# Kernel tuning notes

Hardware: AMD Instinct MI355X
Metric: run time of the kernel (lower is better)

Reference implementation:

```python
import jax, jax.numpy as jnp
import numpy as np

EMBED_DIM = 1024
NUM_HEADS = 16
HEAD_DIM = EMBED_DIM // NUM_HEADS
LN_EPS = 1e-5


def setup_inputs() -> dict:
    key = jax.random.key(0)
    ks = jax.random.split(key, 7)
    B, N, D = 4, 2048, EMBED_DIM
    s = 1.0 / np.sqrt(D)  # ~kaiming-uniform scale for Linear weights
    return {
        "inputs": jax.random.normal(ks[0], (B, N, D), dtype=jnp.float32),
        "W_q": jax.random.uniform(ks[1], (D, D), jnp.float32, -s, s),
        "W_k": jax.random.uniform(ks[2], (D, D), jnp.float32, -s, s),
        "W_v": jax.random.uniform(ks[3], (D, D), jnp.float32, -s, s),
        "W_o": jax.random.uniform(ks[4], (D, D), jnp.float32, -s, s),
        "ln_gamma": jnp.ones((D,), jnp.float32),
        "ln_beta": jnp.zeros((D,), jnp.float32),
    }


def reference(inputs, W_q, W_k, W_v, W_o, ln_gamma, ln_beta):
    x = inputs
    B, N, D = x.shape
    H, Hd = NUM_HEADS, HEAD_DIM
    # torch nn.Linear computes x @ W.T; W_* stored as (out, in)
    q = (x @ W_q.T).reshape(B, N, H, Hd).transpose(0, 2, 1, 3)  # [B,H,N,Hd]
    k = (x @ W_k.T).reshape(B, N, H, Hd).transpose(0, 2, 1, 3)
    v = (x @ W_v.T).reshape(B, N, H, Hd).transpose(0, 2, 1, 3)
    scores = jnp.einsum("bhqd,bhkd->bhqk", q, k) / jnp.sqrt(jnp.float32(Hd))
    attn = jax.nn.softmax(scores, axis=-1)  # dropout p=0 -> identity
    out = jnp.einsum("bhqk,bhkd->bhqd", attn, v)
    out = out.transpose(0, 2, 1, 3).reshape(B, N, D)
    out = out @ W_o.T
    # residual + LayerNorm
    y = out + x
    mu = jnp.mean(y, axis=-1, keepdims=True)
    var = jnp.mean(jnp.square(y - mu), axis=-1, keepdims=True)
    y = (y - mu) * jax.lax.rsqrt(var + LN_EPS)
    return y * ln_gamma + ln_beta
```

## Files before the change

### kernel.cpp

```cpp
#include <hip/hip_runtime.h>
#include <hip/hip_bf16.h>
#include <stdint.h>

typedef __attribute__((ext_vector_type(8))) short bf16x8;
typedef __attribute__((ext_vector_type(4))) float f32x4;

#define GLOBAL_AS __attribute__((address_space(1)))
#define LDS_AS    __attribute__((address_space(3)))

__device__ __forceinline__ void load_lds16(const void* g, void* l) {
  __builtin_amdgcn_global_load_lds((const GLOBAL_AS void*)g, (LDS_AS void*)l, 16, 0, 0);
}

__device__ __forceinline__ float bf2f(short s) {
  return __uint_as_float(((unsigned)(unsigned short)s) << 16);
}
__device__ __forceinline__ short f2bfn(float f) {
  __hip_bfloat16 h = __float2bfloat16(f);
  return __builtin_bit_cast(short, h);
}

__global__ __launch_bounds__(256) void cvt_bf16(const float* __restrict__ in,
                                                short* __restrict__ out, int n) {
  int i = (blockIdx.x * 256 + threadIdx.x) * 8;
  if (i >= n) return;
  float4 a = *(const float4*)(in + i);
  float4 b = *(const float4*)(in + i + 4);
  bf16x8 o;
  o[0] = f2bfn(a.x); o[1] = f2bfn(a.y); o[2] = f2bfn(a.z); o[3] = f2bfn(a.w);
  o[4] = f2bfn(b.x); o[5] = f2bfn(b.y); o[6] = f2bfn(b.z); o[7] = f2bfn(b.w);
  *(bf16x8*)(out + i) = o;
}

__global__ __launch_bounds__(256) void cvt_w(const float* __restrict__ q,
                                             const float* __restrict__ k,
                                             const float* __restrict__ v,
                                             const float* __restrict__ o,
                                             short* __restrict__ Wb,
                                             short* __restrict__ Wob) {
  const int sel = blockIdx.x >> 9;
  const int inner = blockIdx.x & 511;
  const int i = (inner * 256 + threadIdx.x) * 8;
  const float* src = sel == 0 ? q : sel == 1 ? k : sel == 2 ? v : o;
  short* dst = sel == 0 ? Wb : sel == 1 ? Wb + 1024 * 1024
             : sel == 2 ? Wb + 2 * 1024 * 1024 : Wob;
  float4 a = *(const float4*)(src + i);
  float4 b = *(const float4*)(src + i + 4);
  bf16x8 ov;
  ov[0] = f2bfn(a.x); ov[1] = f2bfn(a.y); ov[2] = f2bfn(a.z); ov[3] = f2bfn(a.w);
  ov[4] = f2bfn(b.x); ov[5] = f2bfn(b.y); ov[6] = f2bfn(b.z); ov[7] = f2bfn(b.w);
  *(bf16x8*)(dst + i) = ov;
}

template<int OUT_BF16>
__global__ __launch_bounds__(256) void gemm_bt(const short* __restrict__ A,
                                               const short* __restrict__ B,
                                               void* __restrict__ Cp,
                                               int M, int N, int K) {
  __shared__ short As[128 * 64];
  __shared__ short Bs[128 * 64];
  const int t = threadIdx.x, l = t & 63, w = t >> 6;
  const int g = l >> 4, li = l & 15;
  const int wr = w >> 1, wc = w & 1;
  const int bid = blockIdx.x;
  const int bm = (bid & 7) * 8 + ((bid >> 3) & 7);
  const int bn = bid >> 6;
  f32x4 acc[4][4] = {};
  const size_t arow0 = (size_t)(bm * 128) * K;
  const size_t brow0 = (size_t)(bn * 128) * K;
  for (int k0 = 0; k0 < K; k0 += 64) {
    __syncthreads();
#pragma unroll
    for (int it = 0; it < 4; ++it) {
      int e = it * 2048 + t * 8;
      int r = e >> 6, c = e & 63;
      load_lds16(A + arow0 + (size_t)r * K + (k0 + c), &As[e]);
      load_lds16(B + brow0 + (size_t)r * K + (k0 + c), &Bs[e]);
    }
    __syncthreads();
#pragma unroll
    for (int kk = 0; kk < 2; ++kk) {
      bf16x8 af[4], bfr[4];
#pragma unroll
      for (int m = 0; m < 4; ++m)
        af[m] = *(const bf16x8*)&As[(wr * 64 + m * 16 + li) * 64 + kk * 32 + g * 8];
#pragma unroll
      for (int n = 0; n < 4; ++n)
        bfr[n] = *(const bf16x8*)&Bs[(wc * 64 + n * 16 + li) * 64 + kk * 32 + g * 8];
#pragma unroll
      for (int m = 0; m < 4; ++m)
#pragma unroll
        for (int n = 0; n < 4; ++n)
          acc[m][n] = __builtin_amdgcn_mfma_f32_16x16x32_bf16(af[m], bfr[n], acc[m][n], 0, 0, 0);
    }
  }
#pragma unroll
  for (int m = 0; m < 4; ++m)
#pragma unroll
    for (int n = 0; n < 4; ++n)
#pragma unroll
      for (int r = 0; r < 4; ++r) {
        int row = bm * 128 + wr * 64 + m * 16 + g * 4 + r;
        int col = bn * 128 + wc * 64 + n * 16 + li;
        if (OUT_BF16)
          ((short*)Cp)[(size_t)row * N + col] = f2bfn(acc[m][n][r]);
        else
          ((float*)Cp)[(size_t)row * N + col] = acc[m][n][r];
      }
}

__global__ __launch_bounds__(256) void transpose_v(const short* __restrict__ qkv,
                                                   short* __restrict__ VT) {
  const int kt = blockIdx.x;
  const int bh = blockIdx.y;
  const int b = bh >> 4, h = bh & 15;
  __shared__ short T[64][72];
  const int t = threadIdx.x;
  const size_t src = (size_t)b * 2048 * 3072 + 2048 + (size_t)h * 64;
#pragma unroll
  for (int i = 0; i < 2; ++i) {
    int k = i * 32 + (t >> 3);
    int d0 = (t & 7) * 8;
    bf16x8 v = *(const bf16x8*)(qkv + src + (size_t)(kt * 64 + k) * 3072 + d0);
#pragma unroll
    for (int j = 0; j < 8; ++j) T[d0 + j][k] = v[j];
  }
  __syncthreads();
#pragma unroll
  for (int i = 0; i < 2; ++i) {
    int d = i * 32 + (t >> 3);
    int k0 = (t & 7) * 8;
    bf16x8 v = *(const bf16x8*)&T[d][k0];
    *(bf16x8*)(VT + ((size_t)bh * 64 + d) * 2048 + kt * 64 + k0) = v;
  }
}

__global__ __launch_bounds__(256, 4) void attn_fwd(const short* __restrict__ qkv,
                                                   const short* __restrict__ VT,
                                                   short* __restrict__ obuf) {
  const int f0 = blockIdx.x;
  const int work = (f0 & 7) * 128 + (f0 >> 3);
  const int qt = work & 15;
  const int bh = work >> 4;
  const int b = bh >> 4, h = bh & 15;
  const int t = threadIdx.x, w = t >> 6, l = t & 63;
  const int g = l >> 4, li = l & 15;

  __shared__ short Ks[2][64 * 64];
  __shared__ short Vts[2][64 * 64];
  __shared__ short Ps[4][16 * 64];

  const size_t base = (size_t)b * 2048 * 3072 + (size_t)h * 64;
  const short* Vsrc = VT + (size_t)bh * 64 * 2048;

  bf16x8 qf[2][2];
  {
    const float QSC = 0.125f * 1.44269504088896341f;
#pragma unroll
    for (int qh = 0; qh < 2; ++qh) {
      const short* qp = qkv + base + (size_t)(qt * 128 + w * 32 + qh * 16 + li) * 3072;
#pragma unroll
      for (int c = 0; c < 2; ++c) {
        bf16x8 v = *(const bf16x8*)(qp + c * 32 + g * 8);
#pragma unroll
        for (int i = 0; i < 8; ++i) v[i] = f2bfn(bf2f(v[i]) * QSC);
        qf[qh][c] = v;
      }
    }
  }

  bf16x8 ones;
#pragma unroll
  for (int i = 0; i < 8; ++i) ones[i] = (short)0x3F80;

  float m_[2] = {-1e30f, -1e30f};
  f32x4 o_[2][4], lacc[2];
#pragma unroll
  for (int qh = 0; qh < 2; ++qh) {
#pragma unroll
    for (int dj = 0; dj < 4; ++dj) o_[qh][dj] = (f32x4){0.f, 0.f, 0.f, 0.f};
    lacc[qh] = (f32x4){0.f, 0.f, 0.f, 0.f};
  }

  const int sw = li & 7;

#define STAGE(buf, kt_)                                                          \
  {                                                                              \
    _Pragma("unroll")                                                            \
    for (int it = 0; it < 2; ++it) {                                             \
      int e = it * 2048 + t * 8;                                                 \
      int r = e >> 6;                                                            \
      int cs = (e >> 3) & 7;                                                     \
      int cg = cs ^ (r & 7);                                                     \
      load_lds16(qkv + base + 1024 + (size_t)((kt_) * 64 + r) * 3072 + cg * 8,   \
                 &Ks[buf][e]);                                                   \
      load_lds16(Vsrc + (size_t)r * 2048 + (kt_) * 64 + cg * 8, &Vts[buf][e]);   \
    }                                                                            \
  }

  STAGE(0, 0);
  asm volatile("s_waitcnt vmcnt(0)" ::: "memory");
  __syncthreads();

  for (int kt = 0; kt < 32; ++kt) {
    const int cur = kt & 1;
    if (kt + 1 < 32) STAGE(cur ^ 1, kt + 1);

    f32x4 s_[2][4];
#pragma unroll
    for (int qh = 0; qh < 2; ++qh)
#pragma unroll
      for (int j = 0; j < 4; ++j) s_[qh][j] = (f32x4){0.f, 0.f, 0.f, 0.f};
    __builtin_amdgcn_s_setprio(1);
#pragma unroll
    for (int c = 0; c < 2; ++c)
#pragma unroll
      for (int j = 0; j < 4; ++j) {
        bf16x8 kf = *(const bf16x8*)&Ks[cur][(j * 16 + li) * 64 + (((c * 4 + g) ^ sw) * 8)];
        s_[0][j] = __builtin_amdgcn_mfma_f32_16x16x32_bf16(kf, qf[0][c], s_[0][j], 0, 0, 0);
        s_[1][j] = __builtin_amdgcn_mfma_f32_16x16x32_bf16(kf, qf[1][c], s_[1][j], 0, 0, 0);
      }
    __builtin_amdgcn_s_setprio(0);

    float mt[2];
#pragma unroll
    for (int qh = 0; qh < 2; ++qh) {
      float a0 = fmaxf(fmaxf(s_[qh][0][0], s_[qh][0][1]), s_[qh][0][2]);
      float a1 = fmaxf(fmaxf(s_[qh][0][3], s_[qh][1][0]), s_[qh][1][1]);
      float a2 = fmaxf(fmaxf(s_[qh][1][2], s_[qh][1][3]), s_[qh][2][0]);
      float a3 = fmaxf(fmaxf(s_[qh][2][1], s_[qh][2][2]), s_[qh][2][3]);
      float a4 = fmaxf(fmaxf(s_[qh][3][0], s_[qh][3][1]), s_[qh][3][2]);
      float b0 = fmaxf(fmaxf(a0, a1), a2);
      float b1 = fmaxf(fmaxf(a3, a4), s_[qh][3][3]);
      float m0 = fmaxf(b0, b1);
      m0 = fmaxf(m0, __shfl_xor(m0, 16));
      m0 = fmaxf(m0, __shfl_xor(m0, 32));
      mt[qh] = m0;
    }

    bool ok = (mt[0] <= m_[0] + 8.f) && (mt[1] <= m_[1] + 8.f);
    if (!__all(ok)) {
#pragma unroll
      for (int qh = 0; qh < 2; ++qh) {
        float mn = fmaxf(m_[qh], mt[qh]);
        float al = exp2f(m_[qh] - mn);
        m_[qh] = mn;
#pragma unroll
        for (int r = 0; r < 4; ++r) {
          float alr = __shfl(al, (l & 48) | (g * 4 + r));
#pragma unroll
          for (int dj = 0; dj < 4; ++dj) o_[qh][dj][r] *= alr;
          lacc[qh][r] *= alr;
        }
      }
    }

#pragma unroll
    for (int qh = 0; qh < 2; ++qh) {
#pragma unroll
      for (int j = 0; j < 4; ++j) {
        float p0 = exp2f(s_[qh][j][0] - m_[qh]);
        float p1 = exp2f(s_[qh][j][1] - m_[qh]);
        float p2 = exp2f(s_[qh][j][2] - m_[qh]);
        float p3 = exp2f(s_[qh][j][3] - m_[qh]);
        unsigned u0, u1;
        asm("v_cvt_pk_bf16_f32 %0, %1, %2" : "=v"(u0) : "v"(p0), "v"(p1));
        asm("v_cvt_pk_bf16_f32 %0, %1, %2" : "=v"(u1) : "v"(p2), "v"(p3));
        uint2 pk2; pk2.x = u0; pk2.y = u1;
        int pos = (j * 16 + g * 4) ^ (sw << 3);
        *(uint2*)&Ps[w][li * 64 + pos] = pk2;
      }
      asm volatile("s_waitcnt lgkmcnt(0)" ::: "memory");

      __builtin_amdgcn_s_setprio(1);
#pragma unroll
      for (int c = 0; c < 2; ++c) {
        bf16x8 pa = *(const bf16x8*)&Ps[w][li * 64 + (((c * 4 + g) ^ sw) * 8)];
        lacc[qh] = __builtin_amdgcn_mfma_f32_16x16x32_bf16(pa, ones, lacc[qh], 0, 0, 0);
#pragma unroll
        for (int dj = 0; dj < 4; ++dj) {
          bf16x8 vb = *(const bf16x8*)&Vts[cur][(dj * 16 + li) * 64 + (((c * 4 + g) ^ sw) * 8)];
          o_[qh][dj] = __builtin_amdgcn_mfma_f32_16x16x32_bf16(pa, vb, o_[qh][dj], 0, 0, 0);
        }
      }
      __builtin_amdgcn_s_setprio(0);
    }

    asm volatile("s_waitcnt vmcnt(0)" ::: "memory");
    __syncthreads();
  }

#pragma unroll
  for (int qh = 0; qh < 2; ++qh)
#pragma unroll
    for (int r = 0; r < 4; ++r) {
      float ilr = 1.f / lacc[qh][r];
      int row = b * 2048 + qt * 128 + w * 32 + qh * 16 + g * 4 + r;
#pragma unroll
      for (int dj = 0; dj < 4; ++dj) {
        int col = h * 64 + dj * 16 + li;
        obuf[(size_t)row * 1024 + col] = f2bfn(o_[qh][dj][r] * ilr);
      }
    }
#undef STAGE
}

__global__ __launch_bounds__(256) void resid_ln(const float* __restrict__ U,
                                                const float* __restrict__ x,
                                                const float* __restrict__ gamma,
                                                const float* __restrict__ beta,
                                                float* __restrict__ out) {
  const int row = blockIdx.x;
  const int t = threadIdx.x, w = t >> 6, l = t & 63;
  const float4 uu = *(const float4*)(U + (size_t)row * 1024 + t * 4);
  const float4 xx = *(const float4*)(x + (size_t)row * 1024 + t * 4);
  float y[4] = {uu.x + xx.x, uu.y + xx.y, uu.z + xx.z, uu.w + xx.w};
  float s = (y[0] + y[1]) + (y[2] + y[3]);
#pragma unroll
  for (int d = 1; d < 64; d <<= 1) s += __shfl_xor(s, d);
  __shared__ float red[4];
  if (l == 0) red[w] = s;
  __syncthreads();
  s = red[0] + red[1] + red[2] + red[3];
  const float mu = s * (1.f / 1024.f);
  float vs = 0.f;
#pragma unroll
  for (int i = 0; i < 4; ++i) { float d0 = y[i] - mu; vs += d0 * d0; }
#pragma unroll
  for (int d = 1; d < 64; d <<= 1) vs += __shfl_xor(vs, d);
  __syncthreads();
  if (l == 0) red[w] = vs;
  __syncthreads();
  vs = red[0] + red[1] + red[2] + red[3];
  const float rstd = rsqrtf(vs * (1.f / 1024.f) + 1e-5f);
  const float4 gg = *(const float4*)(gamma + t * 4);
  const float4 bb = *(const float4*)(beta + t * 4);
  float4 oo;
  oo.x = (y[0] - mu) * rstd * gg.x + bb.x;
  oo.y = (y[1] - mu) * rstd * gg.y + bb.y;
  oo.z = (y[2] - mu) * rstd * gg.z + bb.z;
  oo.w = (y[3] - mu) * rstd * gg.w + bb.w;
  *(float4*)(out + (size_t)row * 1024 + t * 4) = oo;
}

extern "C" void kernel_launch(void* const* d_in, const int* in_sizes, int n_in,
                              void* d_out, int out_size, void* d_ws, size_t ws_size,
                              hipStream_t stream) {
  const float* x     = (const float*)d_in[0];
  const float* W_q   = (const float*)d_in[1];
  const float* W_k   = (const float*)d_in[2];
  const float* W_v   = (const float*)d_in[3];
  const float* W_o   = (const float*)d_in[4];
  const float* gamma = (const float*)d_in[5];
  const float* beta  = (const float*)d_in[6];
  float* out = (float*)d_out;

  char* ws = (char*)d_ws;
  short* xb   = (short*)ws;  ws += (size_t)8192 * 1024 * 2;
  short* Wb   = (short*)ws;  ws += (size_t)3072 * 1024 * 2;
  short* Wob  = (short*)ws;  ws += (size_t)1024 * 1024 * 2;
  short* qkv  = (short*)ws;  ws += (size_t)8192 * 3072 * 2;
  short* obuf = (short*)ws;  ws += (size_t)8192 * 1024 * 2;
  float* U    = (float*)ws;  ws += (size_t)8192 * 1024 * 4;
  short* VT   = (short*)U;

  cvt_bf16<<<4096, 256, 0, stream>>>(x, xb, 8192 * 1024);
  cvt_w<<<2048, 256, 0, stream>>>(W_q, W_k, W_v, W_o, Wb, Wob);

  gemm_bt<1><<<1536, 256, 0, stream>>>(xb, Wb, qkv, 8192, 3072, 1024);
  transpose_v<<<dim3(32, 64), 256, 0, stream>>>(qkv, VT);
  attn_fwd<<<1024, 256, 0, stream>>>(qkv, VT, obuf);
  gemm_bt<0><<<512, 256, 0, stream>>>(obuf, Wob, U, 8192, 1024, 1024);
  resid_ln<<<8192, 256, 0, stream>>>(U, x, gamma, beta, out);
}
```

Measured before the change: 262.6 us.

## Load V fragments directly into registers and fold softmax scale into exp

V tiles are no longer staged through LDS. Each wave loads its V MFMA operands straight from global memory into registers at the start of each key tile, which removes the Vts shared buffer and halves LDS use. Separately, Q is no longer pre-scaled and re-rounded to bf16. The scale is applied with an fma inside the exp2 and in the rescale threshold. The trade-off is redundant global/L2 reads of V by all four waves, plus an earlier vmcnt(0) wait that also blocks on the next K prefetch.

After: 472.8 us. 1.8x slower.

```diff
diff --git a/kernel.cpp b/kernel.cpp
--- a/kernel.cpp
+++ b/kernel.cpp
@@ -147,27 +147,22 @@
   const int g = l >> 4, li = l & 15;
 
   __shared__ short Ks[2][64 * 64];
-  __shared__ short Vts[2][64 * 64];
   __shared__ short Ps[4][16 * 64];
 
   const size_t base = (size_t)b * 2048 * 3072 + (size_t)h * 64;
   const short* Vsrc = VT + (size_t)bh * 64 * 2048;
 
   bf16x8 qf[2][2];
-  {
-    const float QSC = 0.125f * 1.44269504088896341f;
-#pragma unroll
-    for (int qh = 0; qh < 2; ++qh) {
-      const short* qp = qkv + base + (size_t)(qt * 128 + w * 32 + qh * 16 + li) * 3072;
-#pragma unroll
-      for (int c = 0; c < 2; ++c) {
-        bf16x8 v = *(const bf16x8*)(qp + c * 32 + g * 8);
-#pragma unroll
-        for (int i = 0; i < 8; ++i) v[i] = f2bfn(bf2f(v[i]) * QSC);
-        qf[qh][c] = v;
-      }
-    }
-  }
+#pragma unroll
+  for (int qh = 0; qh < 2; ++qh) {
+    const short* qp = qkv + base + (size_t)(qt * 128 + w * 32 + qh * 16 + li) * 3072;
+#pragma unroll
+    for (int c = 0; c < 2; ++c)
+      qf[qh][c] = *(const bf16x8*)(qp + c * 32 + g * 8);
+  }
+
+  const float QSC = 0.125f * 1.44269504088896341f;
+  const float THR = 8.0f / QSC;
 
   bf16x8 ones;
 #pragma unroll
@@ -194,7 +189,6 @@
       int cg = cs ^ (r & 7);                                                     \
       load_lds16(qkv + base + 1024 + (size_t)((kt_) * 64 + r) * 3072 + cg * 8,   \
                  &Ks[buf][e]);                                                   \
-      load_lds16(Vsrc + (size_t)r * 2048 + (kt_) * 64 + cg * 8, &Vts[buf][e]);   \
     }                                                                            \
   }
 
@@ -204,6 +198,15 @@
 
   for (int kt = 0; kt < 32; ++kt) {
     const int cur = kt & 1;
+
+    bf16x8 vb[2][4];
+#pragma unroll
+    for (int c = 0; c < 2; ++c)
+#pragma unroll
+      for (int dj = 0; dj < 4; ++dj)
+        vb[c][dj] = *(const bf16x8*)(Vsrc + (size_t)(dj * 16 + li) * 2048 +
+                                     kt * 64 + c * 32 + g * 8);
+
     if (kt + 1 < 32) STAGE(cur ^ 1, kt + 1);
 
     f32x4 s_[2][4];
@@ -238,12 +241,12 @@
       mt[qh] = m0;
     }
 
-    bool ok = (mt[0] <= m_[0] + 8.f) && (mt[1] <= m_[1] + 8.f);
+    bool ok = (mt[0] <= m_[0] + THR) && (mt[1] <= m_[1] + THR);
     if (!__all(ok)) {
 #pragma unroll
       for (int qh = 0; qh < 2; ++qh) {
         float mn = fmaxf(m_[qh], mt[qh]);
-        float al = exp2f(m_[qh] - mn);
+        float al = exp2f((m_[qh] - mn) * QSC);
         m_[qh] = mn;
 #pragma unroll
         for (int r = 0; r < 4; ++r) {
@@ -257,12 +260,13 @@
 
 #pragma unroll
     for (int qh = 0; qh < 2; ++qh) {
+      const float mq = m_[qh] * QSC;
 #pragma unroll
       for (int j = 0; j < 4; ++j) {
-        float p0 = exp2f(s_[qh][j][0] - m_[qh]);
-        float p1 = exp2f(s_[qh][j][1] - m_[qh]);
-        float p2 = exp2f(s_[qh][j][2] - m_[qh]);
-        float p3 = exp2f(s_[qh][j][3] - m_[qh]);
+        float p0 = exp2f(fmaf(s_[qh][j][0], QSC, -mq));
+        float p1 = exp2f(fmaf(s_[qh][j][1], QSC, -mq));
+        float p2 = exp2f(fmaf(s_[qh][j][2], QSC, -mq));
+        float p3 = exp2f(fmaf(s_[qh][j][3], QSC, -mq));
         unsigned u0, u1;
         asm("v_cvt_pk_bf16_f32 %0, %1, %2" : "=v"(u0) : "v"(p0), "v"(p1));
         asm("v_cvt_pk_bf16_f32 %0, %1, %2" : "=v"(u1) : "v"(p2), "v"(p3));
@@ -271,6 +275,7 @@
         *(uint2*)&Ps[w][li * 64 + pos] = pk2;
       }
       asm volatile("s_waitcnt lgkmcnt(0)" ::: "memory");
+      if (qh == 0) asm volatile("s_waitcnt vmcnt(0)" ::: "memory");
 
       __builtin_amdgcn_s_setprio(1);
 #pragma unroll
@@ -278,15 +283,12 @@
         bf16x8 pa = *(const bf16x8*)&Ps[w][li * 64 + (((c * 4 + g) ^ sw) * 8)];
         lacc[qh] = __builtin_amdgcn_mfma_f32_16x16x32_bf16(pa, ones, lacc[qh], 0, 0, 0);
 #pragma unroll
-        for (int dj = 0; dj < 4; ++dj) {
-          bf16x8 vb = *(const bf16x8*)&Vts[cur][(dj * 16 + li) * 64 + (((c * 4 + g) ^ sw) * 8)];
-          o_[qh][dj] = __builtin_amdgcn_mfma_f32_16x16x32_bf16(pa, vb, o_[qh][dj], 0, 0, 0);
-        }
+        for (int dj = 0; dj < 4; ++dj)
+          o_[qh][dj] = __builtin_amdgcn_mfma_f32_16x16x32_bf16(pa, vb[c][dj], o_[qh][dj], 0, 0, 0);
       }
       __builtin_amdgcn_s_setprio(0);
     }
 
-    asm volatile("s_waitcnt vmcnt(0)" ::: "memory");
     __syncthreads();
   }
 
```

## Swizzle GEMM LDS tiles and share V fragments across query halves

Applied to the files above, without the earlier changes.

The GEMM now XOR-swizzles 16-byte column groups in its shared-memory tiles to avoid bank conflicts when MFMA fragments are read. In attention, P gets a separate buffer per query half, so V fragments are loaded once per k-chunk and reused for both halves, halving V LDS reads. This raises shared memory and register use, so occupancy hint drops from 4 to 3 blocks per CU.

New measurement: 238.9 us. -9.0%, faster.

```diff
diff --git a/kernel.cpp b/kernel.cpp
--- a/kernel.cpp
+++ b/kernel.cpp
@@ -12,9 +12,6 @@
   __builtin_amdgcn_global_load_lds((const GLOBAL_AS void*)g, (LDS_AS void*)l, 16, 0, 0);
 }
 
-__device__ __forceinline__ float bf2f(short s) {
-  return __uint_as_float(((unsigned)(unsigned short)s) << 16);
-}
 __device__ __forceinline__ short f2bfn(float f) {
   __hip_bfloat16 h = __float2bfloat16(f);
   return __builtin_bit_cast(short, h);
@@ -65,6 +62,7 @@
   const int bid = blockIdx.x;
   const int bm = (bid & 7) * 8 + ((bid >> 3) & 7);
   const int bn = bid >> 6;
+  const int sw = li & 7;
   f32x4 acc[4][4] = {};
   const size_t arow0 = (size_t)(bm * 128) * K;
   const size_t brow0 = (size_t)(bn * 128) * K;
@@ -73,9 +71,11 @@
 #pragma unroll
     for (int it = 0; it < 4; ++it) {
       int e = it * 2048 + t * 8;
-      int r = e >> 6, c = e & 63;
-      load_lds16(A + arow0 + (size_t)r * K + (k0 + c), &As[e]);
-      load_lds16(B + brow0 + (size_t)r * K + (k0 + c), &Bs[e]);
+      int r = e >> 6;
+      int cs = (e >> 3) & 7;
+      int cg = cs ^ (r & 7);
+      load_lds16(A + arow0 + (size_t)r * K + (k0 + cg * 8), &As[e]);
+      load_lds16(B + brow0 + (size_t)r * K + (k0 + cg * 8), &Bs[e]);
     }
     __syncthreads();
 #pragma unroll
@@ -83,10 +83,10 @@
       bf16x8 af[4], bfr[4];
 #pragma unroll
       for (int m = 0; m < 4; ++m)
-        af[m] = *(const bf16x8*)&As[(wr * 64 + m * 16 + li) * 64 + kk * 32 + g * 8];
+        af[m] = *(const bf16x8*)&As[(wr * 64 + m * 16 + li) * 64 + (((kk * 4 + g) ^ sw) * 8)];
 #pragma unroll
       for (int n = 0; n < 4; ++n)
-        bfr[n] = *(const bf16x8*)&Bs[(wc * 64 + n * 16 + li) * 64 + kk * 32 + g * 8];
+        bfr[n] = *(const bf16x8*)&Bs[(wc * 64 + n * 16 + li) * 64 + (((kk * 4 + g) ^ sw) * 8)];
 #pragma unroll
       for (int m = 0; m < 4; ++m)
 #pragma unroll
@@ -135,7 +135,7 @@
   }
 }
 
-__global__ __launch_bounds__(256, 4) void attn_fwd(const short* __restrict__ qkv,
+__global__ __launch_bounds__(256, 3) void attn_fwd(const short* __restrict__ qkv,
                                                    const short* __restrict__ VT,
                                                    short* __restrict__ obuf) {
   const int f0 = blockIdx.x;
@@ -148,7 +148,7 @@
 
   __shared__ short Ks[2][64 * 64];
   __shared__ short Vts[2][64 * 64];
-  __shared__ short Ps[4][16 * 64];
+  __shared__ short Ps[4][2][16 * 64];
 
   const size_t base = (size_t)b * 2048 * 3072 + (size_t)h * 64;
   const short* Vsrc = VT + (size_t)bh * 64 * 2048;
@@ -163,7 +163,10 @@
       for (int c = 0; c < 2; ++c) {
         bf16x8 v = *(const bf16x8*)(qp + c * 32 + g * 8);
 #pragma unroll
-        for (int i = 0; i < 8; ++i) v[i] = f2bfn(bf2f(v[i]) * QSC);
+        for (int i = 0; i < 8; ++i) {
+          float f = __uint_as_float(((unsigned)(unsigned short)v[i]) << 16);
+          v[i] = f2bfn(f * QSC);
+        }
         qf[qh][c] = v;
       }
     }
@@ -268,23 +271,28 @@
         asm("v_cvt_pk_bf16_f32 %0, %1, %2" : "=v"(u1) : "v"(p2), "v"(p3));
         uint2 pk2; pk2.x = u0; pk2.y = u1;
         int pos = (j * 16 + g * 4) ^ (sw << 3);
-        *(uint2*)&Ps[w][li * 64 + pos] = pk2;
-      }
-      asm volatile("s_waitcnt lgkmcnt(0)" ::: "memory");
-
-      __builtin_amdgcn_s_setprio(1);
-#pragma unroll
-      for (int c = 0; c < 2; ++c) {
-        bf16x8 pa = *(const bf16x8*)&Ps[w][li * 64 + (((c * 4 + g) ^ sw) * 8)];
+        *(uint2*)&Ps[w][qh][li * 64 + pos] = pk2;
+      }
+    }
+    asm volatile("s_waitcnt lgkmcnt(0)" ::: "memory");
+
+    __builtin_amdgcn_s_setprio(1);
+#pragma unroll
+    for (int c = 0; c < 2; ++c) {
+      bf16x8 vb[4];
+#pragma unroll
+      for (int dj = 0; dj < 4; ++dj)
+        vb[dj] = *(const bf16x8*)&Vts[cur][(dj * 16 + li) * 64 + (((c * 4 + g) ^ sw) * 8)];
+#pragma unroll
+      for (int qh = 0; qh < 2; ++qh) {
+        bf16x8 pa = *(const bf16x8*)&Ps[w][qh][li * 64 + (((c * 4 + g) ^ sw) * 8)];
         lacc[qh] = __builtin_amdgcn_mfma_f32_16x16x32_bf16(pa, ones, lacc[qh], 0, 0, 0);
 #pragma unroll
-        for (int dj = 0; dj < 4; ++dj) {
-          bf16x8 vb = *(const bf16x8*)&Vts[cur][(dj * 16 + li) * 64 + (((c * 4 + g) ^ sw) * 8)];
-          o_[qh][dj] = __builtin_amdgcn_mfma_f32_16x16x32_bf16(pa, vb, o_[qh][dj], 0, 0, 0);
-        }
-      }
-      __builtin_amdgcn_s_setprio(0);
-    }
+        for (int dj = 0; dj < 4; ++dj)
+          o_[qh][dj] = __builtin_amdgcn_mfma_f32_16x16x32_bf16(pa, vb[dj], o_[qh][dj], 0, 0, 0);
+      }
+    }
+    __builtin_amdgcn_s_setprio(0);
 
     asm volatile("s_waitcnt vmcnt(0)" ::: "memory");
     __syncthreads();
```
